# Optimization experiments

Measured on AMD Instinct MI355X. Metric: run time of the kernel, lower is better.

Reference implementation:

```python
import jax, jax.numpy as jnp
import numpy as np

V = 1_000_000
D = 128
HS = 128
NUM_GRAPHS = 16384  # static segment count (== batch.max()+1 in the torch code)


def setup_inputs() -> dict:
    key = jax.random.key(0)
    k1, k2, k3, k4, k5 = jax.random.split(key, 5)
    H = jax.random.normal(k1, (V, D), dtype=jnp.float32)
    batch = jnp.sort(jax.random.randint(k2, (V,), 0, NUM_GRAPHS, dtype=jnp.int64))
    # nn.Linear-style init scale
    W_proj = jax.random.normal(k3, (HS, D), dtype=jnp.float32) * (1.0 / np.sqrt(D))
    b_proj = jax.random.normal(k4, (HS,), dtype=jnp.float32) * (1.0 / np.sqrt(D))
    w_score = jax.random.normal(k5, (HS,), dtype=jnp.float32) * (1.0 / np.sqrt(HS))
    return {"H": H, "batch": batch, "W_proj": W_proj, "b_proj": b_proj, "w_score": w_score}


def reference(H, batch, W_proj, b_proj, w_score):
    # e_v = a^T tanh(W h_v)            -> [V]
    e = jnp.tanh(H @ W_proj.T + b_proj) @ w_score
    # per-graph segment softmax (stable: shift by segment max)
    max_per_g = jax.ops.segment_max(e, batch, num_segments=NUM_GRAPHS)  # [G]
    a = jnp.exp(e - max_per_g[batch])
    denom = jax.ops.segment_sum(a, batch, num_segments=NUM_GRAPHS)  # [G]
    alpha = a / jnp.maximum(denom[batch], 1e-12)
    # weighted sum pooling: h_G = sum_v alpha_v h_v  -> [G, D]
    out = jax.ops.segment_sum(alpha[:, None] * H, batch, num_segments=NUM_GRAPHS)
    return out
```

## Files before the change

### kernel.cpp

```cpp
#include <hip/hip_runtime.h>
#include <hip/hip_bf16.h>

typedef __bf16 bf16x8 __attribute__((ext_vector_type(8)));
typedef float f32x4 __attribute__((ext_vector_type(4)));

constexpr int NUM_G = 16384;
constexpr int DIM = 128;
constexpr int CHUNK = 128;

__global__ void seg_starts_kernel(const int* __restrict__ batch, int* __restrict__ seg, int V) {
    int v = blockIdx.x * blockDim.x + threadIdx.x;
    if (v >= V) return;
    int b1 = batch[v];
    int b0 = (v == 0) ? -1 : batch[v - 1];
    for (int g = b0 + 1; g <= b1; ++g) seg[g] = v;
    if (v == V - 1)
        for (int g = b1 + 1; g <= NUM_G; ++g) seg[g] = V;
}

__launch_bounds__(256, 3)
__global__ void attn_agg_kernel(const float* __restrict__ Hm,
                                const float* __restrict__ Wp,
                                const float* __restrict__ bp,
                                const float* __restrict__ wsc,
                                const int* __restrict__ seg,
                                float* __restrict__ out) {
    __shared__ __align__(16) __bf16 Hs[CHUNK * DIM];
    __shared__ float e_part[2][CHUNK];
    __shared__ float alpha_s[CHUNK];
    __shared__ float wsum[2][DIM];
    __shared__ float red[4];

    const int t = threadIdx.x;
    const int lane = t & 63;
    const int wave = t >> 6;
    const int l15 = lane & 15;
    const int lq = lane >> 4;
    const int mgrp = wave >> 1;
    const int nhalf = wave & 1;

    bf16x8 bfrag[4][4];
    float bias_n[4], wsc_n[4];
#pragma unroll
    for (int nt = 0; nt < 4; ++nt) {
        int n_g = (nhalf * 4 + nt) * 16 + l15;
        bias_n[nt] = bp[n_g];
        wsc_n[nt] = wsc[n_g];
#pragma unroll
        for (int ks = 0; ks < 4; ++ks) {
            const float* src = Wp + n_g * DIM + ks * 32 + lq * 8;
            f32x4 w0 = *(const f32x4*)src;
            f32x4 w1 = *(const f32x4*)(src + 4);
            bf16x8 f;
            f[0] = (__bf16)w0[0]; f[1] = (__bf16)w0[1]; f[2] = (__bf16)w0[2]; f[3] = (__bf16)w0[3];
            f[4] = (__bf16)w1[0]; f[5] = (__bf16)w1[1]; f[6] = (__bf16)w1[2]; f[7] = (__bf16)w1[3];
            bfrag[nt][ks] = f;
        }
    }

    const int g = blockIdx.x;
    const int v0 = seg[g];
    const int n = seg[g + 1] - v0;

    const int col = t & 127;
    const int hf = t >> 7;
    const int dch = col >> 3, doff = col & 7;
    float acc = 0.f;
    float lsum = 0.f;

    for (int r0 = 0; r0 < n; r0 += CHUNK) {
        int c = min(CHUNK, n - r0);
        __syncthreads();

        for (int i = t; i < c * 16; i += 256) {
            int row = i >> 4, ch = i & 15;
            const float* src = Hm + (size_t)(v0 + r0 + row) * DIM + ch * 8;
            f32x4 a0 = *(const f32x4*)src;
            f32x4 a1 = *(const f32x4*)(src + 4);
            bf16x8 hv;
            hv[0] = (__bf16)a0[0]; hv[1] = (__bf16)a0[1]; hv[2] = (__bf16)a0[2]; hv[3] = (__bf16)a0[3];
            hv[4] = (__bf16)a1[0]; hv[5] = (__bf16)a1[1]; hv[6] = (__bf16)a1[2]; hv[7] = (__bf16)a1[3];
            int chs = ch ^ (row & 15);
            *(bf16x8*)&Hs[row * DIM + chs * 8] = hv;
        }
        __syncthreads();

#pragma unroll
        for (int mt = 0; mt < 4; ++mt) {
            int mtile = mt * 2 + mgrp;
            if (mtile * 16 < c) {
                int arow = mtile * 16 + l15;
                bf16x8 afrag[4];
#pragma unroll
                for (int ks = 0; ks < 4; ++ks) {
                    int chs = (ks * 4 + lq) ^ l15;
                    afrag[ks] = *(const bf16x8*)&Hs[arow * DIM + chs * 8];
                }
                float epl[4] = {0.f, 0.f, 0.f, 0.f};
#pragma unroll
                for (int nt = 0; nt < 4; ++nt) {
                    f32x4 dacc = {0.f, 0.f, 0.f, 0.f};
#pragma unroll
                    for (int ks = 0; ks < 4; ++ks)
                        dacc = __builtin_amdgcn_mfma_f32_16x16x32_bf16(afrag[ks], bfrag[nt][ks], dacc, 0, 0, 0);
#pragma unroll
                    for (int r = 0; r < 4; ++r) {
                        float x = dacc[r] + bias_n[nt];
                        float ex = __expf(2.f * x);
                        float th = 1.f - 2.f * __builtin_amdgcn_rcpf(ex + 1.f);
                        epl[r] += th * wsc_n[nt];
                    }
                }
#pragma unroll
                for (int m = 1; m < 16; m <<= 1)
#pragma unroll
                    for (int r = 0; r < 4; ++r)
                        epl[r] += __shfl_xor(epl[r], m, 64);
                if (l15 == 0)
#pragma unroll
                    for (int r = 0; r < 4; ++r)
                        e_part[nhalf][mtile * 16 + lq * 4 + r] = epl[r];
            }
        }
        __syncthreads();

        float pv = 0.f;
        if (t < c) {
            float ev = e_part[0][t] + e_part[1][t];
            float p = __expf(ev);
            alpha_s[t] = p;
            pv = p;
        }
#pragma unroll
        for (int m = 1; m < 64; m <<= 1) pv += __shfl_xor(pv, m, 64);
        if (lane == 0) red[wave] = pv;
        __syncthreads();
        lsum += red[0] + red[1] + red[2] + red[3];

        {
            int r = hf;
            for (; r + 6 < c; r += 8) {
                float p0 = alpha_s[r],     p1 = alpha_s[r + 2];
                float p2 = alpha_s[r + 4], p3 = alpha_s[r + 6];
                float h0 = (float)Hs[(r)     * DIM + ((dch ^ ((r)     & 15)) * 8) + doff];
                float h1 = (float)Hs[(r + 2) * DIM + ((dch ^ ((r + 2) & 15)) * 8) + doff];
                float h2 = (float)Hs[(r + 4) * DIM + ((dch ^ ((r + 4) & 15)) * 8) + doff];
                float h3 = (float)Hs[(r + 6) * DIM + ((dch ^ ((r + 6) & 15)) * 8) + doff];
                acc += p0 * h0 + p1 * h1 + p2 * h2 + p3 * h3;
            }
            for (; r < c; r += 2)
                acc += alpha_s[r] * (float)Hs[r * DIM + ((dch ^ (r & 15)) * 8) + doff];
        }
    }

    wsum[hf][col] = acc;
    __syncthreads();
    if (t < 128)
        out[(size_t)g * DIM + t] = (wsum[0][t] + wsum[1][t]) / fmaxf(lsum, 1e-12f);
}

extern "C" void kernel_launch(void* const* d_in, const int* in_sizes, int n_in,
                              void* d_out, int out_size, void* d_ws, size_t ws_size,
                              hipStream_t stream) {
    const float* Hm  = (const float*)d_in[0];
    const int* batch = (const int*)d_in[1];
    const float* Wp  = (const float*)d_in[2];
    const float* bp  = (const float*)d_in[3];
    const float* wsc = (const float*)d_in[4];
    float* out = (float*)d_out;
    int* seg = (int*)d_ws;
    int V = in_sizes[1];

    seg_starts_kernel<<<(V + 255) / 256, 256, 0, stream>>>(batch, seg, V);
    attn_agg_kernel<<<NUM_G, 256, 0, stream>>>(Hm, Wp, bp, wsc, seg, out);
}
```

Baseline: 824.2 us.

## Process multiple graphs per block with smaller chunks and per-wave N split

Each block now loops over 11 consecutive graphs instead of one, so the W_proj fragment load and bf16 conversion is amortised across graphs. The MFMA work is re-split so each wave owns 32 output columns across all row tiles, which halves the B-fragment registers. CHUNK drops to 64 and launch bounds rise to 6 blocks per CU to raise occupancy. The weighted-sum loop now reads bf16 pairs per lane. The grid shrinks to about 1490 blocks, which risks load imbalance and adds per-graph barriers that serialise work within a block.

```diff
diff --git a/kernel.cpp b/kernel.cpp
--- a/kernel.cpp
+++ b/kernel.cpp
@@ -2,11 +2,14 @@
 #include <hip/hip_bf16.h>
 
 typedef __bf16 bf16x8 __attribute__((ext_vector_type(8)));
+typedef __bf16 bf16x2 __attribute__((ext_vector_type(2)));
 typedef float f32x4 __attribute__((ext_vector_type(4)));
 
 constexpr int NUM_G = 16384;
 constexpr int DIM = 128;
-constexpr int CHUNK = 128;
+constexpr int CHUNK = 64;
+constexpr int GPB = 11;
+constexpr int GRID = (NUM_G + GPB - 1) / GPB;
 
 __global__ void seg_starts_kernel(const int* __restrict__ batch, int* __restrict__ seg, int V) {
     int v = blockIdx.x * blockDim.x + threadIdx.x;
@@ -18,7 +21,7 @@
         for (int g = b1 + 1; g <= NUM_G; ++g) seg[g] = V;
 }
 
-__launch_bounds__(256, 3)
+__launch_bounds__(256, 6)
 __global__ void attn_agg_kernel(const float* __restrict__ Hm,
                                 const float* __restrict__ Wp,
                                 const float* __restrict__ bp,
@@ -26,9 +29,9 @@
                                 const int* __restrict__ seg,
                                 float* __restrict__ out) {
     __shared__ __align__(16) __bf16 Hs[CHUNK * DIM];
-    __shared__ float e_part[2][CHUNK];
+    __shared__ float e_part[4][CHUNK];
     __shared__ float alpha_s[CHUNK];
-    __shared__ float wsum[2][DIM];
+    __shared__ float wsum[4][DIM];
     __shared__ float red[4];
 
     const int t = threadIdx.x;
@@ -36,14 +39,12 @@
     const int wave = t >> 6;
     const int l15 = lane & 15;
     const int lq = lane >> 4;
-    const int mgrp = wave >> 1;
-    const int nhalf = wave & 1;
 
-    bf16x8 bfrag[4][4];
-    float bias_n[4], wsc_n[4];
+    bf16x8 bfrag[2][4];
+    float bias_n[2], wsc_n[2];
 #pragma unroll
-    for (int nt = 0; nt < 4; ++nt) {
-        int n_g = (nhalf * 4 + nt) * 16 + l15;
+    for (int nt = 0; nt < 2; ++nt) {
+        int n_g = (wave * 2 + nt) * 16 + l15;
         bias_n[nt] = bp[n_g];
         wsc_n[nt] = wsc[n_g];
 #pragma unroll
@@ -58,105 +59,115 @@
         }
     }
 
-    const int g = blockIdx.x;
-    const int v0 = seg[g];
-    const int n = seg[g + 1] - v0;
+    const int g0 = blockIdx.x * GPB;
+    const int g1 = min(g0 + GPB, NUM_G);
+    if (g0 >= NUM_G) return;
 
-    const int col = t & 127;
-    const int hf = t >> 7;
-    const int dch = col >> 3, doff = col & 7;
-    float acc = 0.f;
-    float lsum = 0.f;
+    const int cp = lane;
+    const int dch = cp >> 2, dof = (cp & 3) * 4;
 
-    for (int r0 = 0; r0 < n; r0 += CHUNK) {
-        int c = min(CHUNK, n - r0);
-        __syncthreads();
+    int s_prev = seg[g0];
+    for (int g = g0; g < g1; ++g) {
+        int s_next = seg[g + 1];
+        int v0 = s_prev;
+        int n = s_next - s_prev;
+        s_prev = s_next;
 
-        for (int i = t; i < c * 16; i += 256) {
-            int row = i >> 4, ch = i & 15;
-            const float* src = Hm + (size_t)(v0 + r0 + row) * DIM + ch * 8;
-            f32x4 a0 = *(const f32x4*)src;
-            f32x4 a1 = *(const f32x4*)(src + 4);
-            bf16x8 hv;
-            hv[0] = (__bf16)a0[0]; hv[1] = (__bf16)a0[1]; hv[2] = (__bf16)a0[2]; hv[3] = (__bf16)a0[3];
-            hv[4] = (__bf16)a1[0]; hv[5] = (__bf16)a1[1]; hv[6] = (__bf16)a1[2]; hv[7] = (__bf16)a1[3];
-            int chs = ch ^ (row & 15);
-            *(bf16x8*)&Hs[row * DIM + chs * 8] = hv;
-        }
-        __syncthreads();
+        float acc0 = 0.f, acc1 = 0.f;
+        float lsum = 0.f;
+
+        for (int r0 = 0; r0 < n; r0 += CHUNK) {
+            int c = min(CHUNK, n - r0);
+            __syncthreads();
+
+            for (int i = t; i < c * 16; i += 256) {
+                int row = i >> 4, ch = i & 15;
+                const float* src = Hm + (size_t)(v0 + r0 + row) * DIM + ch * 8;
+                f32x4 a0 = *(const f32x4*)src;
+                f32x4 a1 = *(const f32x4*)(src + 4);
+                bf16x8 hv;
+                hv[0] = (__bf16)a0[0]; hv[1] = (__bf16)a0[1]; hv[2] = (__bf16)a0[2]; hv[3] = (__bf16)a0[3];
+                hv[4] = (__bf16)a1[0]; hv[5] = (__bf16)a1[1]; hv[6] = (__bf16)a1[2]; hv[7] = (__bf16)a1[3];
+                int chs = ch ^ (row & 15);
+                *(bf16x8*)&Hs[row * DIM + chs * 8] = hv;
+            }
+            __syncthreads();
 
 #pragma unroll
-        for (int mt = 0; mt < 4; ++mt) {
-            int mtile = mt * 2 + mgrp;
-            if (mtile * 16 < c) {
-                int arow = mtile * 16 + l15;
-                bf16x8 afrag[4];
+            for (int mt = 0; mt < 4; ++mt) {
+                if (mt * 16 < c) {
+                    int arow = mt * 16 + l15;
+                    bf16x8 afrag[4];
 #pragma unroll
-                for (int ks = 0; ks < 4; ++ks) {
-                    int chs = (ks * 4 + lq) ^ l15;
-                    afrag[ks] = *(const bf16x8*)&Hs[arow * DIM + chs * 8];
+                    for (int ks = 0; ks < 4; ++ks) {
+                        int chs = (ks * 4 + lq) ^ l15;
+                        afrag[ks] = *(const bf16x8*)&Hs[arow * DIM + chs * 8];
+                    }
+                    float epl[4] = {0.f, 0.f, 0.f, 0.f};
+#pragma unroll
+                    for (int nt = 0; nt < 2; ++nt) {
+                        f32x4 dacc = {0.f, 0.f, 0.f, 0.f};
+#pragma unroll
+                        for (int ks = 0; ks < 4; ++ks)
+                            dacc = __builtin_amdgcn_mfma_f32_16x16x32_bf16(afrag[ks], bfrag[nt][ks], dacc, 0, 0, 0);
+#pragma unroll
+                        for (int r = 0; r < 4; ++r) {
+                            float x = dacc[r] + bias_n[nt];
+                            float ex = __expf(2.f * x);
+                            float th = 1.f - 2.f * __builtin_amdgcn_rcpf(ex + 1.f);
+                            epl[r] += th * wsc_n[nt];
+                        }
+                    }
+#pragma unroll
+                    for (int m = 1; m < 16; m <<= 1)
+#pragma unroll
+                        for (int r = 0; r < 4; ++r)
+                            epl[r] += __shfl_xor(epl[r], m, 64);
+                    if (l15 == 0)
+#pragma unroll
+                        for (int r = 0; r < 4; ++r)
+                            e_part[wave][mt * 16 + lq * 4 + r] = epl[r];
                 }
-                float epl[4] = {0.f, 0.f, 0.f, 0.f};
+            }
+            __syncthreads();
+
+            float pv = 0.f;
+            if (t < c) {
+                float ev = e_part[0][t] + e_part[1][t] + e_part[2][t] + e_part[3][t];
+                float p = __expf(ev);
+                alpha_s[t] = p;
+                pv = p;
+            }
 #pragma unroll
-                for (int nt = 0; nt < 4; ++nt) {
-                    f32x4 dacc = {0.f, 0.f, 0.f, 0.f};
-#pragma unroll
-                    for (int ks = 0; ks < 4; ++ks)
-                        dacc = __builtin_amdgcn_mfma_f32_16x16x32_bf16(afrag[ks], bfrag[nt][ks], dacc, 0, 0, 0);
-#pragma unroll
-                    for (int r = 0; r < 4; ++r) {
-                        float x = dacc[r] + bias_n[nt];
-                        float ex = __expf(2.f * x);
-                        float th = 1.f - 2.f * __builtin_amdgcn_rcpf(ex + 1.f);
-                        epl[r] += th * wsc_n[nt];
-                    }
+            for (int m = 1; m < 64; m <<= 1) pv += __shfl_xor(pv, m, 64);
+            if (lane == 0) red[wave] = pv;
+            __syncthreads();
+            lsum += red[0] + red[1] + red[2] + red[3];
+
+            {
+                int r = wave;
+                for (; r + 4 < c; r += 8) {
+                    float p0 = alpha_s[r], p1 = alpha_s[r + 4];
+                    bf16x2 h0 = *(const bf16x2*)((const char*)&Hs[(r)     * DIM + ((dch ^ ((r)     & 15)) * 8)] + dof);
+                    bf16x2 h1 = *(const bf16x2*)((const char*)&Hs[(r + 4) * DIM + ((dch ^ ((r + 4) & 15)) * 8)] + dof);
+                    acc0 += p0 * (float)h0[0] + p1 * (float)h1[0];
+                    acc1 += p0 * (float)h0[1] + p1 * (float)h1[1];
                 }
-#pragma unroll
-                for (int m = 1; m < 16; m <<= 1)
-#pragma unroll
-                    for (int r = 0; r < 4; ++r)
-                        epl[r] += __shfl_xor(epl[r], m, 64);
-                if (l15 == 0)
-#pragma unroll
-                    for (int r = 0; r < 4; ++r)
-                        e_part[nhalf][mtile * 16 + lq * 4 + r] = epl[r];
+                for (; r < c; r += 4) {
+                    float p = alpha_s[r];
+                    bf16x2 h = *(const bf16x2*)((const char*)&Hs[r * DIM + ((dch ^ (r & 15)) * 8)] + dof);
+                    acc0 += p * (float)h[0];
+                    acc1 += p * (float)h[1];
+                }
             }
         }
+
+        *(float2*)&wsum[wave][cp * 2] = make_float2(acc0, acc1);
         __syncthreads();
-
-        float pv = 0.f;
-        if (t < c) {
-            float ev = e_part[0][t] + e_part[1][t];
-            float p = __expf(ev);
-            alpha_s[t] = p;
-            pv = p;
-        }
-#pragma unroll
-        for (int m = 1; m < 64; m <<= 1) pv += __shfl_xor(pv, m, 64);
-        if (lane == 0) red[wave] = pv;
-        __syncthreads();
-        lsum += red[0] + red[1] + red[2] + red[3];
-
-        {
-            int r = hf;
-            for (; r + 6 < c; r += 8) {
-                float p0 = alpha_s[r],     p1 = alpha_s[r + 2];
-                float p2 = alpha_s[r + 4], p3 = alpha_s[r + 6];
-                float h0 = (float)Hs[(r)     * DIM + ((dch ^ ((r)     & 15)) * 8) + doff];
-                float h1 = (float)Hs[(r + 2) * DIM + ((dch ^ ((r + 2) & 15)) * 8) + doff];
-                float h2 = (float)Hs[(r + 4) * DIM + ((dch ^ ((r + 4) & 15)) * 8) + doff];
-                float h3 = (float)Hs[(r + 6) * DIM + ((dch ^ ((r + 6) & 15)) * 8) + doff];
-                acc += p0 * h0 + p1 * h1 + p2 * h2 + p3 * h3;
-            }
-            for (; r < c; r += 2)
-                acc += alpha_s[r] * (float)Hs[r * DIM + ((dch ^ (r & 15)) * 8) + doff];
-        }
+        if (t < 128)
+            out[(size_t)g * DIM + t] =
+                (wsum[0][t] + wsum[1][t] + wsum[2][t] + wsum[3][t]) / fmaxf(lsum, 1e-12f);
     }
-
-    wsum[hf][col] = acc;
-    __syncthreads();
-    if (t < 128)
-        out[(size_t)g * DIM + t] = (wsum[0][t] + wsum[1][t]) / fmaxf(lsum, 1e-12f);
 }
 
 extern "C" void kernel_launch(void* const* d_in, const int* in_sizes, int n_in,
@@ -172,5 +183,5 @@
     int V = in_sizes[1];
 
     seg_starts_kernel<<<(V + 255) / 256, 256, 0, stream>>>(batch, seg, V);
-    attn_agg_kernel<<<NUM_G, 256, 0, stream>>>(Hm, Wp, bp, wsc, seg, out);
+    attn_agg_kernel<<<GRID, 256, 0, stream>>>(Hm, Wp, bp, wsc, seg, out);
 }
```

New measurement: 697.4 us. 15.4% less time.
